# Kernel optimization log

Hardware: AMD Instinct MI355X
Metric: run time of the kernel (lower is better)

The kernel has to match this reference:

```python
import jax, jax.numpy as jnp
import numpy as np

N_NODES = 20000
N_EDGES = 640000
N_FEATS = 3703
HIDDEN = 50
N_CLASSES = 6
N_KENN_LAYERS = 3
# clause: not C_c(x) OR C_c(y) OR not Cite(x,y)  -> literal signs
SIGNS = np.array([-1.0, 1.0, -1.0], dtype=np.float32)


def setup_inputs() -> dict:
    key = jax.random.key(0)
    ks = jax.random.split(key, 12)
    features = jax.random.normal(ks[0], (N_NODES, N_FEATS), dtype=jnp.float32)
    relations = jax.random.normal(ks[1], (N_EDGES, 1), dtype=jnp.float32)
    sx = jax.random.randint(ks[2], (N_EDGES,), 0, N_NODES)
    sy = jax.random.randint(ks[3], (N_EDGES,), 0, N_NODES)

    def dense(k, fan_in, fan_out):
        return jax.random.normal(k, (fan_in, fan_out), dtype=jnp.float32) / np.sqrt(fan_in).astype(np.float32)

    W1 = dense(ks[4], N_FEATS, HIDDEN); b1 = jnp.zeros((HIDDEN,), jnp.float32)
    W2 = dense(ks[5], HIDDEN, HIDDEN);  b2 = jnp.zeros((HIDDEN,), jnp.float32)
    W3 = dense(ks[6], HIDDEN, HIDDEN);  b3 = jnp.zeros((HIDDEN,), jnp.float32)
    W4 = dense(ks[7], HIDDEN, N_CLASSES); b4 = jnp.zeros((N_CLASSES,), jnp.float32)
    # one learnable clause weight per class-clause, per KENN layer (init 0.5 as in KENN)
    clause_weights = jnp.full((N_KENN_LAYERS, N_CLASSES), 0.5, dtype=jnp.float32)
    return dict(features=features, relations=relations, sx=sx, sy=sy,
                W1=W1, b1=b1, W2=W2, b2=b2, W3=W3, b3=b3, W4=W4, b4=b4,
                clause_weights=clause_weights)


def _kenn_layer(z, relations, sx, sy, cw):
    # z: [N, C]; relations: [E, 1]; cw: [C] clause weights
    n = z.shape[0]
    zx = z[sx]                                   # [E, C] gather head literals
    zy = z[sy]                                   # [E, C] gather tail literals
    rel = jnp.broadcast_to(relations, (relations.shape[0], z.shape[1]))  # [E, C]
    signs = jnp.asarray(SIGNS)
    # signed literal preactivations per clause: [E, C, 3]
    v = jnp.stack([-zx, zy, -rel], axis=-1)
    # KENN boost: delta = w_c * softmax(signed preacts) * sign
    d = cw[None, :, None] * jax.nn.softmax(v, axis=-1) * signs[None, None, :]
    # scatter unary deltas back to nodes (relation delta is discarded)
    dz = jax.ops.segment_sum(d[..., 0], sx, num_segments=n)
    dz = dz + jax.ops.segment_sum(d[..., 1], sy, num_segments=n)
    return z + dz


def reference(features, relations, sx, sy, W1, b1, W2, b2, W3, b3, W4, b4, clause_weights):
    # MLP preactivations (dropout inactive at inference)
    x = jax.nn.relu(features @ W1 + b1)
    x = jax.nn.relu(x @ W2 + b2)
    x = jax.nn.relu(x @ W3 + b3)
    z = x @ W4 + b4                               # [N, 6]
    for i in range(N_KENN_LAYERS):
        z = _kenn_layer(z, relations, sx, sy, clause_weights[i])
    return jax.nn.softmax(z, axis=-1)
```

## Files before the change

kernel.cpp:

```cpp
#include <hip/hip_runtime.h>

#define M_NODES 20000
#define K_FEATS 3703
#define PADK 3712
#define NH 50
#define NC 6
#define N_EDGES_C 640000
#define NKB 116

typedef __attribute__((ext_vector_type(8))) __bf16 bf16x8;
typedef __attribute__((ext_vector_type(4))) float f32x4;

__global__ void k_packB(const float* __restrict__ W1, unsigned short* __restrict__ Bh,
                        unsigned short* __restrict__ Bl) {
  int idx = blockIdx.x * 256 + threadIdx.x;
  if (idx >= NKB * 4 * 64 * 8) return;
  int j = idx & 7;
  int lane = (idx >> 3) & 63;
  int t = (idx >> 9) & 3;
  int kb = idx >> 11;
  int k = kb * 32 + (lane >> 4) * 8 + j;
  int c = t * 16 + (lane & 15);
  float v = (k < K_FEATS && c < NH) ? W1[k * NH + c] : 0.f;
  __bf16 hb = (__bf16)v;
  float hf = (float)hb;
  __bf16 lb = (__bf16)(v - hf);
  Bh[idx] = *(unsigned short*)&hb;
  Bl[idx] = *(unsigned short*)&lb;
}

__global__ __launch_bounds__(256) void k_gemm1(const float* __restrict__ A,
    const unsigned short* __restrict__ Bph, const unsigned short* __restrict__ Bpl,
    float* __restrict__ part, int KS) {
  const int lane = threadIdx.x & 63;
  const int w = threadIdx.x >> 6;
  const int row0 = blockIdx.x * 128 + w * 32;
  const int s = blockIdx.y;
  const int ks = s * KS;
  const int ke = (ks + KS < PADK) ? ks + KS : PADK;
  const int nsteps = (ke - ks) >> 5;
  const int g = lane >> 4;
  const int rl = lane & 15;
  const int r0c = min(row0 + rl, M_NODES - 1);
  const int r1c = min(row0 + 16 + rl, M_NODES - 1);
  const float* a0p = A + (size_t)r0c * K_FEATS + 8 * g;
  const float* a1p = A + (size_t)r1c * K_FEATS + 8 * g;
  const bf16x8* BH = (const bf16x8*)Bph;
  const bf16x8* BL = (const bf16x8*)Bpl;

  f32x4 acc[2][4];
  #pragma unroll
  for (int i = 0; i < 2; ++i)
    #pragma unroll
    for (int t = 0; t < 4; ++t) acc[i][t] = (f32x4){0.f, 0.f, 0.f, 0.f};

  #define LOADA(d0, d1, k0) {                                     \
    d0[0] = *(const float4*)(a0p + (k0));                         \
    d0[1] = *(const float4*)(a0p + (k0) + 4);                     \
    d1[0] = *(const float4*)(a1p + (k0));                         \
    d1[1] = *(const float4*)(a1p + (k0) + 4); }
  #define LOADAG(d0, d1, k0) {                                    \
    _Pragma("unroll") for (int j = 0; j < 8; ++j) {               \
      int gk = (k0) + 8 * g + j;                                  \
      float v0 = (gk < K_FEATS) ? a0p[(k0) + j] : 0.f;            \
      float v1 = (gk < K_FEATS) ? a1p[(k0) + j] : 0.f;            \
      ((float*)d0)[j] = v0; ((float*)d1)[j] = v1; } }

  #define BODY(sa0, sa1, k0) {                                    \
    const int kb4 = ((k0) >> 5) * 4;                              \
    bf16x8 bh0 = BH[(kb4 + 0) * 64 + lane];                       \
    bf16x8 bh1 = BH[(kb4 + 1) * 64 + lane];                       \
    bf16x8 bh2 = BH[(kb4 + 2) * 64 + lane];                       \
    bf16x8 bh3 = BH[(kb4 + 3) * 64 + lane];                       \
    bf16x8 bl0 = BL[(kb4 + 0) * 64 + lane];                       \
    bf16x8 bl1 = BL[(kb4 + 1) * 64 + lane];                       \
    bf16x8 bl2 = BL[(kb4 + 2) * 64 + lane];                       \
    bf16x8 bl3 = BL[(kb4 + 3) * 64 + lane];                       \
    bf16x8 ah0, al0, ah1, al1;                                    \
    _Pragma("unroll") for (int j = 0; j < 8; ++j) {               \
      float xv = ((const float*)sa0)[j];                          \
      __bf16 hb = (__bf16)xv; float hf = (float)hb;               \
      ah0[j] = hb; al0[j] = (__bf16)(xv - hf);                    \
      float yv = ((const float*)sa1)[j];                          \
      __bf16 hb2 = (__bf16)yv; float hf2 = (float)hb2;            \
      ah1[j] = hb2; al1[j] = (__bf16)(yv - hf2);                  \
    }                                                             \
    acc[0][0] = __builtin_amdgcn_mfma_f32_16x16x32_bf16(ah0, bh0, acc[0][0], 0, 0, 0); \
    acc[0][1] = __builtin_amdgcn_mfma_f32_16x16x32_bf16(ah0, bh1, acc[0][1], 0, 0, 0); \
    acc[0][2] = __builtin_amdgcn_mfma_f32_16x16x32_bf16(ah0, bh2, acc[0][2], 0, 0, 0); \
    acc[0][3] = __builtin_amdgcn_mfma_f32_16x16x32_bf16(ah0, bh3, acc[0][3], 0, 0, 0); \
    acc[1][0] = __builtin_amdgcn_mfma_f32_16x16x32_bf16(ah1, bh0, acc[1][0], 0, 0, 0); \
    acc[1][1] = __builtin_amdgcn_mfma_f32_16x16x32_bf16(ah1, bh1, acc[1][1], 0, 0, 0); \
    acc[1][2] = __builtin_amdgcn_mfma_f32_16x16x32_bf16(ah1, bh2, acc[1][2], 0, 0, 0); \
    acc[1][3] = __builtin_amdgcn_mfma_f32_16x16x32_bf16(ah1, bh3, acc[1][3], 0, 0, 0); \
    acc[0][0] = __builtin_amdgcn_mfma_f32_16x16x32_bf16(al0, bh0, acc[0][0], 0, 0, 0); \
    acc[0][1] = __builtin_amdgcn_mfma_f32_16x16x32_bf16(al0, bh1, acc[0][1], 0, 0, 0); \
    acc[0][2] = __builtin_amdgcn_mfma_f32_16x16x32_bf16(al0, bh2, acc[0][2], 0, 0, 0); \
    acc[0][3] = __builtin_amdgcn_mfma_f32_16x16x32_bf16(al0, bh3, acc[0][3], 0, 0, 0); \
    acc[1][0] = __builtin_amdgcn_mfma_f32_16x16x32_bf16(al1, bh0, acc[1][0], 0, 0, 0); \
    acc[1][1] = __builtin_amdgcn_mfma_f32_16x16x32_bf16(al1, bh1, acc[1][1], 0, 0, 0); \
    acc[1][2] = __builtin_amdgcn_mfma_f32_16x16x32_bf16(al1, bh2, acc[1][2], 0, 0, 0); \
    acc[1][3] = __builtin_amdgcn_mfma_f32_16x16x32_bf16(al1, bh3, acc[1][3], 0, 0, 0); \
    acc[0][0] = __builtin_amdgcn_mfma_f32_16x16x32_bf16(ah0, bl0, acc[0][0], 0, 0, 0); \
    acc[0][1] = __builtin_amdgcn_mfma_f32_16x16x32_bf16(ah0, bl1, acc[0][1], 0, 0, 0); \
    acc[0][2] = __builtin_amdgcn_mfma_f32_16x16x32_bf16(ah0, bl2, acc[0][2], 0, 0, 0); \
    acc[0][3] = __builtin_amdgcn_mfma_f32_16x16x32_bf16(ah0, bl3, acc[0][3], 0, 0, 0); \
    acc[1][0] = __builtin_amdgcn_mfma_f32_16x16x32_bf16(ah1, bl0, acc[1][0], 0, 0, 0); \
    acc[1][1] = __builtin_amdgcn_mfma_f32_16x16x32_bf16(ah1, bl1, acc[1][1], 0, 0, 0); \
    acc[1][2] = __builtin_amdgcn_mfma_f32_16x16x32_bf16(ah1, bl2, acc[1][2], 0, 0, 0); \
    acc[1][3] = __builtin_amdgcn_mfma_f32_16x16x32_bf16(ah1, bl3, acc[1][3], 0, 0, 0); }

  float4 xa0[2], xa1[2], ya0[2], ya1[2];
  LOADA(xa0, xa1, ks);
  for (int t2 = 0; t2 < nsteps; t2 += 2) {
    const int k0 = ks + (t2 << 5);
    const int k1 = k0 + 32;
    if (k1 + 32 > K_FEATS) { LOADAG(ya0, ya1, k1); } else { LOADA(ya0, ya1, k1); }
    BODY(xa0, xa1, k0);
    if (t2 + 2 < nsteps) {
      const int k2 = k0 + 64;
      if (k2 + 32 > K_FEATS) { LOADAG(xa0, xa1, k2); } else { LOADA(xa0, xa1, k2); }
    }
    BODY(ya0, ya1, k1);
  }
  #undef LOADA
  #undef LOADAG
  #undef BODY

  float* p = part + (size_t)s * 1000000;
  #pragma unroll
  for (int i = 0; i < 2; ++i) {
    #pragma unroll
    for (int t = 0; t < 4; ++t) {
      int col = t * 16 + rl;
      if (col < NH) {
        int rowb = row0 + i * 16 + g * 4;
        f32x4 v = acc[i][t];
        #pragma unroll
        for (int q = 0; q < 4; ++q) {
          int row = rowb + q;
          if (row < M_NODES) p[row * NH + col] = v[q];
        }
      }
    }
  }
}

__global__ void k_epi(const float* __restrict__ part, const float* __restrict__ b1,
                      float* __restrict__ x1, int S) {
  int i = blockIdx.x * 256 + threadIdx.x;
  if (i >= M_NODES * NH) return;
  float v = b1[i % NH];
  for (int s = 0; s < S; ++s) v += part[(size_t)s * 1000000 + i];
  x1[i] = fmaxf(v, 0.f);
}

__global__ __launch_bounds__(256) void k_mlp(const float* __restrict__ x1,
    const float* __restrict__ W2, const float* __restrict__ b2,
    const float* __restrict__ W3, const float* __restrict__ b3,
    const float* __restrict__ W4, const float* __restrict__ b4,
    float* __restrict__ z) {
  __shared__ float lX[32 * 51];
  __shared__ float lW2[50 * 52];
  __shared__ float lW3[50 * 52];
  __shared__ float lW4[50 * 8];
  const int tid = threadIdx.x;
  const int row0 = blockIdx.x * 32;
  for (int idx = tid; idx < 2500; idx += 256) {
    int k = idx / 50, n = idx % 50;
    lW2[k * 52 + n] = W2[idx];
    lW3[k * 52 + n] = W3[idx];
  }
  for (int idx = tid; idx < 300; idx += 256) {
    int k = idx / 6, n = idx % 6;
    lW4[k * 8 + n] = W4[idx];
  }
  for (int idx = tid; idx < 1600; idx += 256) {
    int r = idx / 50, k = idx % 50;
    int gr = row0 + r;
    lX[r * 51 + k] = (gr < M_NODES) ? x1[gr * 50 + k] : 0.f;
  }
  __syncthreads();
  const int r = tid >> 3, cg = tid & 7;
  float x[50];
  #pragma unroll
  for (int k = 0; k < 50; ++k) x[k] = lX[r * 51 + k];

  for (int layer = 0; layer < 2; ++layer) {
    const float* lW = (layer == 0) ? lW2 : lW3;
    const float* bg = (layer == 0) ? b2 : b3;
    float acc[7];
    #pragma unroll
    for (int j = 0; j < 7; ++j) {
      int n = cg + 8 * j;
      acc[j] = (n < 50) ? bg[n] : 0.f;
    }
    #pragma unroll
    for (int k = 0; k < 50; ++k) {
      float xk = x[k];
      #pragma unroll
      for (int j = 0; j < 7; ++j) {
        int n = cg + 8 * j;
        if (n < 50) acc[j] = fmaf(xk, lW[k * 52 + n], acc[j]);
      }
    }
    __syncthreads();
    #pragma unroll
    for (int j = 0; j < 7; ++j) {
      int n = cg + 8 * j;
      if (n < 50) lX[r * 51 + n] = fmaxf(acc[j], 0.f);
    }
    __syncthreads();
    #pragma unroll
    for (int k = 0; k < 50; ++k) x[k] = lX[r * 51 + k];
  }
  if (cg < 6) {
    float accz = b4[cg];
    #pragma unroll
    for (int k = 0; k < 50; ++k) accz = fmaf(x[k], lW4[k * 8 + cg], accz);
    int gr = row0 + r;
    if (gr < M_NODES) z[gr * 6 + cg] = accz;
  }
}

__global__ void k_count(const int* __restrict__ sx, const int* __restrict__ sy,
                        int* __restrict__ cnt) {
  int e = blockIdx.x * 256 + threadIdx.x;
  if (e >= N_EDGES_C) return;
  atomicAdd(&cnt[sx[e]], 1);
  atomicAdd(&cnt[sy[e]], 1);
}

__global__ __launch_bounds__(1024) void k_scan(const int* __restrict__ cnt,
                                               int* __restrict__ off,
                                               int* __restrict__ cur) {
  __shared__ int sums[1024];
  int t = threadIdx.x;
  int base = t * 20;
  int local[20];
  int s = 0;
  #pragma unroll
  for (int j = 0; j < 20; ++j) {
    int idx = base + j;
    int v = (idx < M_NODES) ? cnt[idx] : 0;
    local[j] = s;
    s += v;
  }
  sums[t] = s;
  __syncthreads();
  for (int d = 1; d < 1024; d <<= 1) {
    int v = (t >= d) ? sums[t - d] : 0;
    __syncthreads();
    sums[t] += v;
    __syncthreads();
  }
  int excl = sums[t] - s;
  #pragma unroll
  for (int j = 0; j < 20; ++j) {
    int idx = base + j;
    if (idx < M_NODES) {
      int o = excl + local[j];
      off[idx] = o;
      cur[idx] = o;
    }
  }
  if (t == 1023) off[M_NODES] = sums[1023];
}

__global__ void k_scatter(const int* __restrict__ sx, const int* __restrict__ sy,
                          const float* __restrict__ rel,
                          int* __restrict__ cur, int2* __restrict__ ent) {
  int e = blockIdx.x * 256 + threadIdx.x;
  if (e >= N_EDGES_C) return;
  int a = sx[e], b = sy[e];
  int rb = __float_as_int(rel[e]);
  int p = atomicAdd(&cur[a], 1);
  ent[p] = make_int2((b << 1), rb);
  int q = atomicAdd(&cur[b], 1);
  ent[q] = make_int2((a << 1) | 1, rb);
}

__global__ __launch_bounds__(256) void k_gather(const float* __restrict__ z,
    const int* __restrict__ off, const int2* __restrict__ ent,
    const float* __restrict__ cw, float* __restrict__ partial) {
  int t = blockIdx.x * 256 + threadIdx.x;
  if (t >= M_NODES * 8) return;
  int s = t & 7;
  int n = t >> 3;
  int o0 = off[n];
  int deg = off[n + 1] - o0;
  int lo = o0 + ((deg * s) >> 3);
  int hi = o0 + ((deg * (s + 1)) >> 3);

  const float2* zr = (const float2*)(z + n * 6);
  float2 a0 = zr[0], a1 = zr[1], a2 = zr[2];
  float znv[6] = {a0.x, a0.y, a1.x, a1.y, a2.x, a2.y};
  float w[6];
  #pragma unroll
  for (int c = 0; c < 6; ++c) w[c] = cw[c];
  float dz[6] = {0.f, 0.f, 0.f, 0.f, 0.f, 0.f};

  for (int i = lo; i < hi; ++i) {
    int2 e2 = ent[i];
    int partner = e2.x >> 1;
    int side = e2.x & 1;
    float r = __int_as_float(e2.y);
    const float2* zp2 = (const float2*)(z + partner * 6);
    float2 p0 = zp2[0], p1 = zp2[1], p2 = zp2[2];
    float zpv[6] = {p0.x, p0.y, p1.x, p1.y, p2.x, p2.y};
    float v2 = -r;
    #pragma unroll
    for (int c = 0; c < 6; ++c) {
      float zx = side ? zpv[c] : znv[c];
      float zy = side ? znv[c] : zpv[c];
      float v0 = -zx, v1 = zy;
      float m = fmaxf(fmaxf(v0, v1), v2);
      float e0 = __expf(v0 - m);
      float e1 = __expf(v1 - m);
      float e2v = __expf(v2 - m);
      float inv = w[c] / (e0 + e1 + e2v);
      dz[c] += (side ? e1 : -e0) * inv;
    }
  }
  float* pp = partial + (size_t)s * 120000 + n * 6;
  #pragma unroll
  for (int c = 0; c < 6; ++c) pp[c] = dz[c];
}

__global__ void k_combine(const float* __restrict__ zc, const float* __restrict__ partial,
                          float* __restrict__ zn) {
  int i = blockIdx.x * 256 + threadIdx.x;
  if (i >= M_NODES * NC) return;
  float v = zc[i];
  #pragma unroll
  for (int s = 0; s < 8; ++s) v += partial[(size_t)s * 120000 + i];
  zn[i] = v;
}

__global__ void k_softmax(const float* __restrict__ z, float* __restrict__ out) {
  int i = blockIdx.x * 256 + threadIdx.x;
  if (i >= M_NODES) return;
  const float2* z2 = (const float2*)(z + i * 6);
  float2 p0 = z2[0], p1 = z2[1], p2 = z2[2];
  float v[6] = {p0.x, p0.y, p1.x, p1.y, p2.x, p2.y};
  float m = v[0];
  #pragma unroll
  for (int c = 1; c < 6; ++c) m = fmaxf(m, v[c]);
  float sum = 0.f, ev[6];
  #pragma unroll
  for (int c = 0; c < 6; ++c) { ev[c] = __expf(v[c] - m); sum += ev[c]; }
  float inv = 1.f / sum;
  float2* o2 = (float2*)(out + i * 6);
  o2[0] = make_float2(ev[0] * inv, ev[1] * inv);
  o2[1] = make_float2(ev[2] * inv, ev[3] * inv);
  o2[2] = make_float2(ev[4] * inv, ev[5] * inv);
}

extern "C" void kernel_launch(void* const* d_in, const int* in_sizes, int n_in,
                              void* d_out, int out_size, void* d_ws, size_t ws_size,
                              hipStream_t stream) {
  const float* A   = (const float*)d_in[0];
  const float* rel = (const float*)d_in[1];
  const int*   sx  = (const int*)d_in[2];
  const int*   sy  = (const int*)d_in[3];
  const float* W1  = (const float*)d_in[4];
  const float* b1  = (const float*)d_in[5];
  const float* W2  = (const float*)d_in[6];
  const float* b2  = (const float*)d_in[7];
  const float* W3  = (const float*)d_in[8];
  const float* b3  = (const float*)d_in[9];
  const float* W4  = (const float*)d_in[10];
  const float* b4  = (const float*)d_in[11];
  const float* cw  = (const float*)d_in[12];

  const int S = 8, KS = 512;

  float* base = (float*)d_ws;
  float* part = base;
  float* x1   = base + 8000000;
  float* zA   = base + 9000000;
  float* zB   = base + 9120000;
  unsigned short* Bph = (unsigned short*)(base + 9240000);
  unsigned short* Bpl = (unsigned short*)(base + 9360000);

  int*  cnt  = (int*)base;
  int*  off  = (int*)base + 24576;
  int*  cur  = (int*)base + 49152;
  int2* ent  = (int2*)((int*)base + 73728);
  float* partial = base + 2700000;

  k_packB<<<(NKB * 4 * 64 * 8 + 255) / 256, 256, 0, stream>>>(W1, Bph, Bpl);
  k_gemm1<<<dim3(157, S), 256, 0, stream>>>(A, Bph, Bpl, part, KS);
  k_epi<<<(M_NODES * NH + 255) / 256, 256, 0, stream>>>(part, b1, x1, S);
  k_mlp<<<(M_NODES + 31) / 32, 256, 0, stream>>>(x1, W2, b2, W3, b3, W4, b4, zA);

  hipMemsetAsync(cnt, 0, (M_NODES + 1) * sizeof(int), stream);
  k_count<<<(N_EDGES_C + 255) / 256, 256, 0, stream>>>(sx, sy, cnt);
  k_scan<<<1, 1024, 0, stream>>>(cnt, off, cur);
  k_scatter<<<(N_EDGES_C + 255) / 256, 256, 0, stream>>>(sx, sy, rel, cur, ent);

  float* zc = zA;
  float* zn = zB;
  for (int l = 0; l < 3; ++l) {
    k_gather<<<(M_NODES * 8 + 255) / 256, 256, 0, stream>>>(zc, off, ent, cw + 6 * l, partial);
    k_combine<<<(M_NODES * NC + 255) / 256, 256, 0, stream>>>(zc, partial, zn);
    float* t = zc; zc = zn; zn = t;
  }
  k_softmax<<<(M_NODES + 255) / 256, 256, 0, stream>>>(zc, (float*)d_out);
}
```

Before: 357.1 us.

## Prefetch B fragments, fuse epilogue into MLP, pad z to 8, fuse final softmax

Several changes land together. The GEMM now double-buffers the packed W1 bf16 fragments into registers alongside the A prefetch. The split-K reduction, bias and ReLU move from a separate kernel into the MLP's LDS load, so the x1 buffer is no longer written and read back. The KENN state is padded to 8 floats per node for float4 loads and stores, the gather thread mapping becomes slice-major, and the last combine is fused with the output softmax. These cut launches and memory traffic, at the cost of higher register pressure in the GEMM and MLP blocks doing the split-K sums redundantly.

New measurement: 379.3 us. +6.2%, slower.

```diff
diff --git a/kernel.cpp b/kernel.cpp
--- a/kernel.cpp
+++ b/kernel.cpp
@@ -65,17 +65,18 @@
       float v0 = (gk < K_FEATS) ? a0p[(k0) + j] : 0.f;            \
       float v1 = (gk < K_FEATS) ? a1p[(k0) + j] : 0.f;            \
       ((float*)d0)[j] = v0; ((float*)d1)[j] = v1; } }
-
-  #define BODY(sa0, sa1, k0) {                                    \
+  #define LOADB(bh, bl, k0) {                                     \
     const int kb4 = ((k0) >> 5) * 4;                              \
-    bf16x8 bh0 = BH[(kb4 + 0) * 64 + lane];                       \
-    bf16x8 bh1 = BH[(kb4 + 1) * 64 + lane];                       \
-    bf16x8 bh2 = BH[(kb4 + 2) * 64 + lane];                       \
-    bf16x8 bh3 = BH[(kb4 + 3) * 64 + lane];                       \
-    bf16x8 bl0 = BL[(kb4 + 0) * 64 + lane];                       \
-    bf16x8 bl1 = BL[(kb4 + 1) * 64 + lane];                       \
-    bf16x8 bl2 = BL[(kb4 + 2) * 64 + lane];                       \
-    bf16x8 bl3 = BL[(kb4 + 3) * 64 + lane];                       \
+    bh[0] = BH[(kb4 + 0) * 64 + lane];                            \
+    bh[1] = BH[(kb4 + 1) * 64 + lane];                            \
+    bh[2] = BH[(kb4 + 2) * 64 + lane];                            \
+    bh[3] = BH[(kb4 + 3) * 64 + lane];                            \
+    bl[0] = BL[(kb4 + 0) * 64 + lane];                            \
+    bl[1] = BL[(kb4 + 1) * 64 + lane];                            \
+    bl[2] = BL[(kb4 + 2) * 64 + lane];                            \
+    bl[3] = BL[(kb4 + 3) * 64 + lane]; }
+
+  #define BODY(sa0, sa1, bh, bl) {                                \
     bf16x8 ah0, al0, ah1, al1;                                    \
     _Pragma("unroll") for (int j = 0; j < 8; ++j) {               \
       float xv = ((const float*)sa0)[j];                          \
@@ -85,46 +86,51 @@
       __bf16 hb2 = (__bf16)yv; float hf2 = (float)hb2;            \
       ah1[j] = hb2; al1[j] = (__bf16)(yv - hf2);                  \
     }                                                             \
-    acc[0][0] = __builtin_amdgcn_mfma_f32_16x16x32_bf16(ah0, bh0, acc[0][0], 0, 0, 0); \
-    acc[0][1] = __builtin_amdgcn_mfma_f32_16x16x32_bf16(ah0, bh1, acc[0][1], 0, 0, 0); \
-    acc[0][2] = __builtin_amdgcn_mfma_f32_16x16x32_bf16(ah0, bh2, acc[0][2], 0, 0, 0); \
-    acc[0][3] = __builtin_amdgcn_mfma_f32_16x16x32_bf16(ah0, bh3, acc[0][3], 0, 0, 0); \
-    acc[1][0] = __builtin_amdgcn_mfma_f32_16x16x32_bf16(ah1, bh0, acc[1][0], 0, 0, 0); \
-    acc[1][1] = __builtin_amdgcn_mfma_f32_16x16x32_bf16(ah1, bh1, acc[1][1], 0, 0, 0); \
-    acc[1][2] = __builtin_amdgcn_mfma_f32_16x16x32_bf16(ah1, bh2, acc[1][2], 0, 0, 0); \
-    acc[1][3] = __builtin_amdgcn_mfma_f32_16x16x32_bf16(ah1, bh3, acc[1][3], 0, 0, 0); \
-    acc[0][0] = __builtin_amdgcn_mfma_f32_16x16x32_bf16(al0, bh0, acc[0][0], 0, 0, 0); \
-    acc[0][1] = __builtin_amdgcn_mfma_f32_16x16x32_bf16(al0, bh1, acc[0][1], 0, 0, 0); \
-    acc[0][2] = __builtin_amdgcn_mfma_f32_16x16x32_bf16(al0, bh2, acc[0][2], 0, 0, 0); \
-    acc[0][3] = __builtin_amdgcn_mfma_f32_16x16x32_bf16(al0, bh3, acc[0][3], 0, 0, 0); \
-    acc[1][0] = __builtin_amdgcn_mfma_f32_16x16x32_bf16(al1, bh0, acc[1][0], 0, 0, 0); \
-    acc[1][1] = __builtin_amdgcn_mfma_f32_16x16x32_bf16(al1, bh1, acc[1][1], 0, 0, 0); \
-    acc[1][2] = __builtin_amdgcn_mfma_f32_16x16x32_bf16(al1, bh2, acc[1][2], 0, 0, 0); \
-    acc[1][3] = __builtin_amdgcn_mfma_f32_16x16x32_bf16(al1, bh3, acc[1][3], 0, 0, 0); \
-    acc[0][0] = __builtin_amdgcn_mfma_f32_16x16x32_bf16(ah0, bl0, acc[0][0], 0, 0, 0); \
-    acc[0][1] = __builtin_amdgcn_mfma_f32_16x16x32_bf16(ah0, bl1, acc[0][1], 0, 0, 0); \
-    acc[0][2] = __builtin_amdgcn_mfma_f32_16x16x32_bf16(ah0, bl2, acc[0][2], 0, 0, 0); \
-    acc[0][3] = __builtin_amdgcn_mfma_f32_16x16x32_bf16(ah0, bl3, acc[0][3], 0, 0, 0); \
-    acc[1][0] = __builtin_amdgcn_mfma_f32_16x16x32_bf16(ah1, bl0, acc[1][0], 0, 0, 0); \
-    acc[1][1] = __builtin_amdgcn_mfma_f32_16x16x32_bf16(ah1, bl1, acc[1][1], 0, 0, 0); \
-    acc[1][2] = __builtin_amdgcn_mfma_f32_16x16x32_bf16(ah1, bl2, acc[1][2], 0, 0, 0); \
-    acc[1][3] = __builtin_amdgcn_mfma_f32_16x16x32_bf16(ah1, bl3, acc[1][3], 0, 0, 0); }
+    acc[0][0] = __builtin_amdgcn_mfma_f32_16x16x32_bf16(ah0, bh[0], acc[0][0], 0, 0, 0); \
+    acc[0][1] = __builtin_amdgcn_mfma_f32_16x16x32_bf16(ah0, bh[1], acc[0][1], 0, 0, 0); \
+    acc[0][2] = __builtin_amdgcn_mfma_f32_16x16x32_bf16(ah0, bh[2], acc[0][2], 0, 0, 0); \
+    acc[0][3] = __builtin_amdgcn_mfma_f32_16x16x32_bf16(ah0, bh[3], acc[0][3], 0, 0, 0); \
+    acc[1][0] = __builtin_amdgcn_mfma_f32_16x16x32_bf16(ah1, bh[0], acc[1][0], 0, 0, 0); \
+    acc[1][1] = __builtin_amdgcn_mfma_f32_16x16x32_bf16(ah1, bh[1], acc[1][1], 0, 0, 0); \
+    acc[1][2] = __builtin_amdgcn_mfma_f32_16x16x32_bf16(ah1, bh[2], acc[1][2], 0, 0, 0); \
+    acc[1][3] = __builtin_amdgcn_mfma_f32_16x16x32_bf16(ah1, bh[3], acc[1][3], 0, 0, 0); \
+    acc[0][0] = __builtin_amdgcn_mfma_f32_16x16x32_bf16(al0, bh[0], acc[0][0], 0, 0, 0); \
+    acc[0][1] = __builtin_amdgcn_mfma_f32_16x16x32_bf16(al0, bh[1], acc[0][1], 0, 0, 0); \
+    acc[0][2] = __builtin_amdgcn_mfma_f32_16x16x32_bf16(al0, bh[2], acc[0][2], 0, 0, 0); \
+    acc[0][3] = __builtin_amdgcn_mfma_f32_16x16x32_bf16(al0, bh[3], acc[0][3], 0, 0, 0); \
+    acc[1][0] = __builtin_amdgcn_mfma_f32_16x16x32_bf16(al1, bh[0], acc[1][0], 0, 0, 0); \
+    acc[1][1] = __builtin_amdgcn_mfma_f32_16x16x32_bf16(al1, bh[1], acc[1][1], 0, 0, 0); \
+    acc[1][2] = __builtin_amdgcn_mfma_f32_16x16x32_bf16(al1, bh[2], acc[1][2], 0, 0, 0); \
+    acc[1][3] = __builtin_amdgcn_mfma_f32_16x16x32_bf16(al1, bh[3], acc[1][3], 0, 0, 0); \
+    acc[0][0] = __builtin_amdgcn_mfma_f32_16x16x32_bf16(ah0, bl[0], acc[0][0], 0, 0, 0); \
+    acc[0][1] = __builtin_amdgcn_mfma_f32_16x16x32_bf16(ah0, bl[1], acc[0][1], 0, 0, 0); \
+    acc[0][2] = __builtin_amdgcn_mfma_f32_16x16x32_bf16(ah0, bl[2], acc[0][2], 0, 0, 0); \
+    acc[0][3] = __builtin_amdgcn_mfma_f32_16x16x32_bf16(ah0, bl[3], acc[0][3], 0, 0, 0); \
+    acc[1][0] = __builtin_amdgcn_mfma_f32_16x16x32_bf16(ah1, bl[0], acc[1][0], 0, 0, 0); \
+    acc[1][1] = __builtin_amdgcn_mfma_f32_16x16x32_bf16(ah1, bl[1], acc[1][1], 0, 0, 0); \
+    acc[1][2] = __builtin_amdgcn_mfma_f32_16x16x32_bf16(ah1, bl[2], acc[1][2], 0, 0, 0); \
+    acc[1][3] = __builtin_amdgcn_mfma_f32_16x16x32_bf16(ah1, bl[3], acc[1][3], 0, 0, 0); }
 
   float4 xa0[2], xa1[2], ya0[2], ya1[2];
+  bf16x8 xbh[4], xbl[4], ybh[4], ybl[4];
   LOADA(xa0, xa1, ks);
+  LOADB(xbh, xbl, ks);
   for (int t2 = 0; t2 < nsteps; t2 += 2) {
     const int k0 = ks + (t2 << 5);
     const int k1 = k0 + 32;
     if (k1 + 32 > K_FEATS) { LOADAG(ya0, ya1, k1); } else { LOADA(ya0, ya1, k1); }
-    BODY(xa0, xa1, k0);
+    LOADB(ybh, ybl, k1);
+    BODY(xa0, xa1, xbh, xbl);
     if (t2 + 2 < nsteps) {
       const int k2 = k0 + 64;
       if (k2 + 32 > K_FEATS) { LOADAG(xa0, xa1, k2); } else { LOADA(xa0, xa1, k2); }
-    }
-    BODY(ya0, ya1, k1);
+      LOADB(xbh, xbl, k2);
+    }
+    BODY(ya0, ya1, ybh, ybl);
   }
   #undef LOADA
   #undef LOADAG
+  #undef LOADB
   #undef BODY
 
   float* p = part + (size_t)s * 1000000;
@@ -146,20 +152,12 @@
   }
 }
 
-__global__ void k_epi(const float* __restrict__ part, const float* __restrict__ b1,
-                      float* __restrict__ x1, int S) {
-  int i = blockIdx.x * 256 + threadIdx.x;
-  if (i >= M_NODES * NH) return;
-  float v = b1[i % NH];
-  for (int s = 0; s < S; ++s) v += part[(size_t)s * 1000000 + i];
-  x1[i] = fmaxf(v, 0.f);
-}
-
-__global__ __launch_bounds__(256) void k_mlp(const float* __restrict__ x1,
+__global__ __launch_bounds__(256) void k_mlp(const float* __restrict__ part,
+    const float* __restrict__ b1,
     const float* __restrict__ W2, const float* __restrict__ b2,
     const float* __restrict__ W3, const float* __restrict__ b3,
     const float* __restrict__ W4, const float* __restrict__ b4,
-    float* __restrict__ z) {
+    float* __restrict__ z, int S) {
   __shared__ float lX[32 * 51];
   __shared__ float lW2[50 * 52];
   __shared__ float lW3[50 * 52];
@@ -178,7 +176,14 @@
   for (int idx = tid; idx < 1600; idx += 256) {
     int r = idx / 50, k = idx % 50;
     int gr = row0 + r;
-    lX[r * 51 + k] = (gr < M_NODES) ? x1[gr * 50 + k] : 0.f;
+    float v = 0.f;
+    if (gr < M_NODES) {
+      v = b1[k];
+      int o = gr * 50 + k;
+      for (int s = 0; s < S; ++s) v += part[(size_t)s * 1000000 + o];
+      v = fmaxf(v, 0.f);
+    }
+    lX[r * 51 + k] = v;
   }
   __syncthreads();
   const int r = tid >> 3, cg = tid & 7;
@@ -214,12 +219,16 @@
     #pragma unroll
     for (int k = 0; k < 50; ++k) x[k] = lX[r * 51 + k];
   }
-  if (cg < 6) {
-    float accz = b4[cg];
-    #pragma unroll
-    for (int k = 0; k < 50; ++k) accz = fmaf(x[k], lW4[k * 8 + cg], accz);
-    int gr = row0 + r;
-    if (gr < M_NODES) z[gr * 6 + cg] = accz;
+  int gr = row0 + r;
+  if (gr < M_NODES) {
+    if (cg < 6) {
+      float accz = b4[cg];
+      #pragma unroll
+      for (int k = 0; k < 50; ++k) accz = fmaf(x[k], lW4[k * 8 + cg], accz);
+      z[gr * 8 + cg] = accz;
+    } else {
+      z[gr * 8 + cg] = 0.f;
+    }
   }
 }
 
@@ -285,16 +294,16 @@
     const float* __restrict__ cw, float* __restrict__ partial) {
   int t = blockIdx.x * 256 + threadIdx.x;
   if (t >= M_NODES * 8) return;
-  int s = t & 7;
-  int n = t >> 3;
+  int s = t / M_NODES;
+  int n = t - s * M_NODES;
   int o0 = off[n];
   int deg = off[n + 1] - o0;
   int lo = o0 + ((deg * s) >> 3);
   int hi = o0 + ((deg * (s + 1)) >> 3);
 
-  const float2* zr = (const float2*)(z + n * 6);
-  float2 a0 = zr[0], a1 = zr[1], a2 = zr[2];
-  float znv[6] = {a0.x, a0.y, a1.x, a1.y, a2.x, a2.y};
+  const float4* zr4 = (const float4*)(z + n * 8);
+  float4 q0 = zr4[0], q1 = zr4[1];
+  float znv[6] = {q0.x, q0.y, q0.z, q0.w, q1.x, q1.y};
   float w[6];
   #pragma unroll
   for (int c = 0; c < 6; ++c) w[c] = cw[c];
@@ -305,9 +314,9 @@
     int partner = e2.x >> 1;
     int side = e2.x & 1;
     float r = __int_as_float(e2.y);
-    const float2* zp2 = (const float2*)(z + partner * 6);
-    float2 p0 = zp2[0], p1 = zp2[1], p2 = zp2[2];
-    float zpv[6] = {p0.x, p0.y, p1.x, p1.y, p2.x, p2.y};
+    const float4* zp4 = (const float4*)(z + partner * 8);
+    float4 p0 = zp4[0], p1 = zp4[1];
+    float zpv[6] = {p0.x, p0.y, p0.z, p0.w, p1.x, p1.y};
     float v2 = -r;
     #pragma unroll
     for (int c = 0; c < 6; ++c) {
@@ -322,27 +331,45 @@
       dz[c] += (side ? e1 : -e0) * inv;
     }
   }
-  float* pp = partial + (size_t)s * 120000 + n * 6;
-  #pragma unroll
-  for (int c = 0; c < 6; ++c) pp[c] = dz[c];
+  float4* pp = (float4*)(partial + (size_t)s * 160000 + n * 8);
+  pp[0] = make_float4(dz[0], dz[1], dz[2], dz[3]);
+  pp[1] = make_float4(dz[4], dz[5], 0.f, 0.f);
 }
 
 __global__ void k_combine(const float* __restrict__ zc, const float* __restrict__ partial,
                           float* __restrict__ zn) {
-  int i = blockIdx.x * 256 + threadIdx.x;
-  if (i >= M_NODES * NC) return;
-  float v = zc[i];
-  #pragma unroll
-  for (int s = 0; s < 8; ++s) v += partial[(size_t)s * 120000 + i];
-  zn[i] = v;
-}
-
-__global__ void k_softmax(const float* __restrict__ z, float* __restrict__ out) {
-  int i = blockIdx.x * 256 + threadIdx.x;
-  if (i >= M_NODES) return;
-  const float2* z2 = (const float2*)(z + i * 6);
-  float2 p0 = z2[0], p1 = z2[1], p2 = z2[2];
-  float v[6] = {p0.x, p0.y, p1.x, p1.y, p2.x, p2.y};
+  int n = blockIdx.x * 256 + threadIdx.x;
+  if (n >= M_NODES) return;
+  const float4* zr4 = (const float4*)(zc + n * 8);
+  float4 q0 = zr4[0], q1 = zr4[1];
+  float v[6] = {q0.x, q0.y, q0.z, q0.w, q1.x, q1.y};
+  #pragma unroll
+  for (int s = 0; s < 8; ++s) {
+    const float4* pp = (const float4*)(partial + (size_t)s * 160000 + n * 8);
+    float4 a = pp[0], b = pp[1];
+    v[0] += a.x; v[1] += a.y; v[2] += a.z; v[3] += a.w;
+    v[4] += b.x; v[5] += b.y;
+  }
+  float4* o4 = (float4*)(zn + n * 8);
+  o4[0] = make_float4(v[0], v[1], v[2], v[3]);
+  o4[1] = make_float4(v[4], v[5], 0.f, 0.f);
+}
+
+__global__ void k_combine_softmax(const float* __restrict__ zc,
+                                  const float* __restrict__ partial,
+                                  float* __restrict__ out) {
+  int n = blockIdx.x * 256 + threadIdx.x;
+  if (n >= M_NODES) return;
+  const float4* zr4 = (const float4*)(zc + n * 8);
+  float4 q0 = zr4[0], q1 = zr4[1];
+  float v[6] = {q0.x, q0.y, q0.z, q0.w, q1.x, q1.y};
+  #pragma unroll
+  for (int s = 0; s < 8; ++s) {
+    const float4* pp = (const float4*)(partial + (size_t)s * 160000 + n * 8);
+    float4 a = pp[0], b = pp[1];
+    v[0] += a.x; v[1] += a.y; v[2] += a.z; v[3] += a.w;
+    v[4] += b.x; v[5] += b.y;
+  }
   float m = v[0];
   #pragma unroll
   for (int c = 1; c < 6; ++c) m = fmaxf(m, v[c]);
@@ -350,7 +377,7 @@
   #pragma unroll
   for (int c = 0; c < 6; ++c) { ev[c] = __expf(v[c] - m); sum += ev[c]; }
   float inv = 1.f / sum;
-  float2* o2 = (float2*)(out + i * 6);
+  float2* o2 = (float2*)(out + n * 6);
   o2[0] = make_float2(ev[0] * inv, ev[1] * inv);
   o2[1] = make_float2(ev[2] * inv, ev[3] * inv);
   o2[2] = make_float2(ev[4] * inv, ev[5] * inv);
@@ -377,11 +404,10 @@
 
   float* base = (float*)d_ws;
   float* part = base;
-  float* x1   = base + 8000000;
-  float* zA   = base + 9000000;
-  float* zB   = base + 9120000;
-  unsigned short* Bph = (unsigned short*)(base + 9240000);
-  unsigned short* Bpl = (unsigned short*)(base + 9360000);
+  float* zA   = base + 8000000;
+  float* zB   = base + 8160000;
+  unsigned short* Bph = (unsigned short*)(base + 8320000);
+  unsigned short* Bpl = (unsigned short*)(base + 8438784);
 
   int*  cnt  = (int*)base;
   int*  off  = (int*)base + 24576;
@@ -391,8 +417,7 @@
 
   k_packB<<<(NKB * 4 * 64 * 8 + 255) / 256, 256, 0, stream>>>(W1, Bph, Bpl);
   k_gemm1<<<dim3(157, S), 256, 0, stream>>>(A, Bph, Bpl, part, KS);
-  k_epi<<<(M_NODES * NH + 255) / 256, 256, 0, stream>>>(part, b1, x1, S);
-  k_mlp<<<(M_NODES + 31) / 32, 256, 0, stream>>>(x1, W2, b2, W3, b3, W4, b4, zA);
+  k_mlp<<<(M_NODES + 31) / 32, 256, 0, stream>>>(part, b1, W2, b2, W3, b3, W4, b4, zA, S);
 
   hipMemsetAsync(cnt, 0, (M_NODES + 1) * sizeof(int), stream);
   k_count<<<(N_EDGES_C + 255) / 256, 256, 0, stream>>>(sx, sy, cnt);
@@ -403,8 +428,11 @@
   float* zn = zB;
   for (int l = 0; l < 3; ++l) {
     k_gather<<<(M_NODES * 8 + 255) / 256, 256, 0, stream>>>(zc, off, ent, cw + 6 * l, partial);
-    k_combine<<<(M_NODES * NC + 255) / 256, 256, 0, stream>>>(zc, partial, zn);
-    float* t = zc; zc = zn; zn = t;
-  }
-  k_softmax<<<(M_NODES + 255) / 256, 256, 0, stream>>>(zc, (float*)d_out);
-}
+    if (l < 2) {
+      k_combine<<<(M_NODES + 255) / 256, 256, 0, stream>>>(zc, partial, zn);
+      float* t = zc; zc = zn; zn = t;
+    } else {
+      k_combine_softmax<<<(M_NODES + 255) / 256, 256, 0, stream>>>(zc, partial, (float*)d_out);
+    }
+  }
+}
```
